# Kernel tuning notes

Hardware: AMD Instinct MI355X
Metric: run time of the kernel (lower is better)

The kernel has to match this reference:

```python
import jax, jax.numpy as jnp
import numpy as np

B, NSP, H, W = 8, 1024, 256, 256   # frames, superpixels/frame, label-map size
N = B * NSP                        # total superpixel nodes
MIX = 0.5                          # mixing_coeff
SIGMA = 0.05


def _interp_axis(x, out, axis):
    # 1-D bilinear interpolation along `axis`, align_corners=True
    n = x.shape[axis]
    pos = jnp.linspace(0.0, n - 1.0, out).astype(x.dtype)
    i0 = jnp.floor(pos).astype(jnp.int32)
    i1 = jnp.minimum(i0 + 1, n - 1)
    wt = pos - i0.astype(x.dtype)
    shp = [1] * x.ndim
    shp[axis] = out
    wt = wt.reshape(shp)
    return jnp.take(x, i0, axis=axis) * (1 - wt) + jnp.take(x, i1, axis=axis) * wt


def _upsample_ac(x, oh, ow):
    # nn.UpsamplingBilinear2d (align_corners=True)
    if x.shape[2] == oh and x.shape[3] == ow:
        return x
    return _interp_axis(_interp_axis(x, oh, 2), ow, 3)


def _sp_pool(feats, seg):
    # upsample [B,C,h,w] to label resolution, then average features per superpixel -> [N, C]
    C = feats.shape[1]
    up = _upsample_ac(feats, H, W)
    vals = up.transpose(0, 2, 3, 1).reshape(-1, C)          # [B*H*W, C]
    sums = jax.ops.segment_sum(vals, seg, num_segments=N)
    cnt = jax.ops.segment_sum(jnp.ones((seg.shape[0],), vals.dtype), seg, num_segments=N)
    return sums / jnp.maximum(cnt, 1.0)[:, None]


def _gcn(x, Wm, b, src, dst, ew):
    # GCNConv(normalize=False): out_i = sum_{j->i} ew * (x_j @ W) + b
    h = x @ Wm
    agg = jax.ops.segment_sum(h[src] * ew[:, None], dst, num_segments=x.shape[0])
    return agg + b


def _coord_map():
    # channel 0 varies along dim2 (w), channel 1 varies along dim3 (h), both in [0,1]
    c0 = jnp.broadcast_to((jnp.arange(H, dtype=jnp.float32) / (H - 1))[:, None], (H, W))
    c1 = jnp.broadcast_to((jnp.arange(W, dtype=jnp.float32) / (W - 1))[None, :], (H, W))
    return jnp.broadcast_to(jnp.stack([c0, c1], 0)[None], (B, 2, H, W))


def setup_inputs() -> dict:
    key = jax.random.key(0)
    ks = jax.random.split(key, 12)
    labels = jax.random.randint(ks[0], (B, 1, H, W), 0, NSP, dtype=jnp.int32)
    skip0 = jax.random.normal(ks[1], (B, 512, 32, 32), jnp.float32)
    skip1 = jax.random.normal(ks[2], (B, 256, 64, 64), jnp.float32)
    skip2 = jax.random.normal(ks[3], (B, 256, 128, 128), jnp.float32)
    E = 131072
    edges_nn = jax.random.randint(ks[4], (2, E), 0, N, dtype=jnp.int32)
    negs = jax.random.randint(ks[5], (E,), 0, N, dtype=jnp.int32)
    W0 = jax.random.normal(ks[6], (512, 256), jnp.float32) / np.float32(np.sqrt(512))
    W1 = jax.random.normal(ks[7], (256, 256), jnp.float32) / np.float32(np.sqrt(256))
    W2 = jax.random.normal(ks[8], (256, 256), jnp.float32) / np.float32(np.sqrt(256))
    lin_w = jax.random.normal(ks[9], (256, 1), jnp.float32) / np.float32(np.sqrt(256))
    z = jnp.zeros((256,), jnp.float32)
    return {"labels": labels, "skip0": skip0, "skip1": skip1, "skip2": skip2,
            "edges_nn": edges_nn, "negs": negs,
            "W0": W0, "b0": z, "W1": W1, "b1": z, "W2": W2, "b2": z, "lin_w": lin_w}


def reference(labels, skip0, skip1, skip2, edges_nn, negs, W0, b0, W1, b1, W2, b2, lin_w):
    # per-pixel global superpixel id (offset per frame)
    seg = (labels.reshape(B, -1) + NSP * jnp.arange(B, dtype=labels.dtype)[:, None]).reshape(-1)
    src, dst = edges_nn[0], edges_nn[1]

    # pooled normalized coordinates per superpixel -> gaussian edge weights
    pc = _sp_pool(_coord_map(), seg)                        # [N, 2]
    dr = pc[src] - pc[dst]
    dist = jnp.linalg.norm(dr, axis=1)
    edge_attr = jnp.exp(-dist ** 2 / SIGMA)

    x = _sp_pool(skip0, seg)                                # [N, 512]
    layers = [(W0, b0, None), (W1, b1, skip1), (W2, b2, skip2)]
    for i, (Wm, b, sk) in enumerate(layers):
        if i > 0:
            x = (1 - MIX) * x + MIX * _sp_pool(sk, seg)
        x = jax.nn.relu(_gcn(x, Wm, b, src, dst, edge_attr))

    s = x @ lin_w                                           # [N, 1]
    dap = jax.nn.sigmoid(s[src] - s[dst])
    dan = jax.nn.sigmoid(s[src] - s[negs])
    return dan, dap, edge_attr
```

## Files before the change

kernel.cpp:

```cpp
#include <hip/hip_runtime.h>
#include <hip/hip_bf16.h>
#include <cstdint>
#include <cstddef>

#define BB 8
#define NSPX 1024
#define NNODE 8192
#define EE 131072
#define NPIX 524288
#define CH 256

using bf16 = __hip_bfloat16;
typedef unsigned int uint;
typedef unsigned long long u64;

__device__ __forceinline__ float blo(uint u) { return __uint_as_float(u << 16); }
__device__ __forceinline__ float bhi(uint u) { return __uint_as_float(u & 0xffff0000u); }
__device__ __forceinline__ uint packbf2(float a, float b) {
  __hip_bfloat162 h = __float22bfloat162_rn(make_float2(a, b));
  return *reinterpret_cast<uint*>(&h);
}

__global__ __launch_bounds__(256) void zero_kernel(int4* p, int n4) {
  int i = blockIdx.x * 256 + threadIdx.x;
  int stride = gridDim.x * 256;
  int4 z = make_int4(0, 0, 0, 0);
  for (; i < n4; i += stride) p[i] = z;
}

__global__ __launch_bounds__(256) void cnt2_kernel(const int* __restrict__ labels,
                                                   const int* __restrict__ edst,
                                                   int* __restrict__ segb,
                                                   u64* __restrict__ packed,
                                                   int* __restrict__ cnt_e) {
  int blk = blockIdx.x;
  int t = threadIdx.x;
  if (blk < 2048) {
    int p = blk * 256 + t;
    int b = p >> 16;
    int h = (p >> 8) & 255;
    int w = p & 255;
    int seg = labels[p] + (b << 10);
    segb[p] = seg;
    u64 enc = (1ULL << 48) | ((u64)h << 24) | (u64)w;
    atomicAdd(&packed[seg], enc);
  } else {
    int e = (blk - 2048) * 256 + t;
    atomicAdd(&cnt_e[edst[e]], 1);
  }
}

__global__ __launch_bounds__(1024) void scan2_kernel(const u64* __restrict__ packed,
                                                     const int* __restrict__ cnt_e,
                                                     int* __restrict__ poff, int* __restrict__ eoff) {
  __shared__ int ps[1024];
  int which = blockIdx.x;
  int* coff = which ? eoff : poff;
  int t = threadIdx.x;
  int base = t * 8;
  int v[8];
  int sum = 0;
#pragma unroll
  for (int i = 0; i < 8; ++i) {
    int x = which ? cnt_e[base + i] : (int)(packed[base + i] >> 48);
    v[i] = sum;
    sum += x;
  }
  ps[t] = sum;
  __syncthreads();
  for (int off = 1; off < 1024; off <<= 1) {
    int x = (t >= off) ? ps[t - off] : 0;
    __syncthreads();
    ps[t] += x;
    __syncthreads();
  }
  int prev = (t == 0) ? 0 : ps[t - 1];
#pragma unroll
  for (int i = 0; i < 8; ++i) coff[base + i] = prev + v[i];
  if (t == 1023) coff[8192] = ps[1023];
}

__global__ __launch_bounds__(256) void rcnt_kernel(const u64* __restrict__ packed,
                                                   float* __restrict__ rcnt,
                                                   float* __restrict__ pch, float* __restrict__ pcw) {
  int n = blockIdx.x * 256 + threadIdx.x;
  if (n >= NNODE) return;
  u64 v = packed[n];
  int c = (int)(v >> 48);
  int sh = (int)((v >> 24) & 0xFFFFFF);
  int sw = (int)(v & 0xFFFFFF);
  float r = 1.0f / (float)(c > 1 ? c : 1);
  rcnt[n] = r;
  pch[n] = (float)sh * r * (1.0f / 255.0f);
  pcw[n] = (float)sw * r * (1.0f / 255.0f);
}

__global__ __launch_bounds__(256) void scatter2_kernel(const int* __restrict__ segb,
                                                       const int* __restrict__ poff,
                                                       int* __restrict__ pcur,
                                                       int* __restrict__ psorted,
                                                       const int* __restrict__ esrc,
                                                       const int* __restrict__ edst,
                                                       const float* __restrict__ pch,
                                                       const float* __restrict__ pcw,
                                                       const int* __restrict__ eoff,
                                                       int* __restrict__ ecur,
                                                       uint2* __restrict__ evw,
                                                       float* __restrict__ outp) {
  int blk = blockIdx.x;
  int t = threadIdx.x;
  if (blk < 2048) {
    int p = blk * 256 + t;
    int s = segb[p];
    int pos = poff[s] + atomicAdd(&pcur[s], 1);
    psorted[pos] = p;
  } else {
    int e = (blk - 2048) * 256 + t;
    int s1 = esrc[e], d1 = edst[e];
    float dh = pch[s1] - pch[d1];
    float dw = pcw[s1] - pcw[d1];
    float ea = expf(-(dh * dh + dw * dw) * 20.0f);
    outp[2 * EE + e] = ea;
    int pos = eoff[d1] + atomicAdd(&ecur[d1], 1);
    evw[pos] = make_uint2((uint)s1, __float_as_uint(ea));
  }
}

__global__ __launch_bounds__(256) void gemm_kmaj_bf16(const float* __restrict__ A,
                                                      const float* __restrict__ W,
                                                      bf16* __restrict__ out) {
  __shared__ float As[64][36];
  int b = blockIdx.z;
  int m0 = blockIdx.x * 32;
  int n0 = blockIdx.y * 128;
  int t = threadIdx.x;
  int ct = t & 31;
  int rm = t >> 5;
  int l8 = t & 7, kr = t >> 3;
  const float* Ab = A + (size_t)b * 512 * 1024;
  float4 acc[4];
#pragma unroll
  for (int i = 0; i < 4; ++i) acc[i] = make_float4(0.f, 0.f, 0.f, 0.f);
  for (int k0 = 0; k0 < 512; k0 += 64) {
#pragma unroll
    for (int pass = 0; pass < 2; ++pass) {
      int k = kr + pass * 32;
      float4 v = *(const float4*)&Ab[(size_t)(k0 + k) * 1024 + m0 + l8 * 4];
      *(float4*)&As[k][l8 * 4] = v;
    }
    __syncthreads();
#pragma unroll 8
    for (int k = 0; k < 64; ++k) {
      float4 a = *(const float4*)&As[k][rm * 4];
      float4 wv = *(const float4*)&W[(size_t)(k0 + k) * 256 + n0 + ct * 4];
      acc[0].x += a.x * wv.x; acc[0].y += a.x * wv.y; acc[0].z += a.x * wv.z; acc[0].w += a.x * wv.w;
      acc[1].x += a.y * wv.x; acc[1].y += a.y * wv.y; acc[1].z += a.y * wv.z; acc[1].w += a.y * wv.w;
      acc[2].x += a.z * wv.x; acc[2].y += a.z * wv.y; acc[2].z += a.z * wv.z; acc[2].w += a.z * wv.w;
      acc[3].x += a.w * wv.x; acc[3].y += a.w * wv.y; acc[3].z += a.w * wv.z; acc[3].w += a.w * wv.w;
    }
    __syncthreads();
  }
#pragma unroll
  for (int i = 0; i < 4; ++i) {
    int m = m0 + rm * 4 + i;
    uint2 pk = make_uint2(packbf2(acc[i].x, acc[i].y), packbf2(acc[i].z, acc[i].w));
    *(uint2*)&out[((size_t)b * 1024 + m) * 256 + n0 + ct * 4] = pk;
  }
}

__global__ __launch_bounds__(256) void transpose64_bf16(const float* __restrict__ src, bf16* __restrict__ dst,
                                                        int C, int P) {
  __shared__ float tile[64][65];
  int b = blockIdx.z;
  int p0 = blockIdx.x * 64;
  int c0 = blockIdx.y * 64;
  int t = threadIdx.x;
  int l16 = t & 15, r16 = t >> 4;
#pragma unroll
  for (int pass = 0; pass < 4; ++pass) {
    int c = r16 + pass * 16;
    float4 v = *(const float4*)&src[((size_t)b * C + c0 + c) * P + p0 + l16 * 4];
    tile[c][l16 * 4 + 0] = v.x;
    tile[c][l16 * 4 + 1] = v.y;
    tile[c][l16 * 4 + 2] = v.z;
    tile[c][l16 * 4 + 3] = v.w;
  }
  __syncthreads();
  int l8 = t & 7, r32 = t >> 3;
#pragma unroll
  for (int pass = 0; pass < 2; ++pass) {
    int p = r32 + pass * 32;
    uint r[4];
#pragma unroll
    for (int q = 0; q < 4; ++q)
      r[q] = packbf2(tile[l8 * 8 + 2 * q][p], tile[l8 * 8 + 2 * q + 1][p]);
    *(uint4*)&dst[((size_t)b * P + p0 + p) * C + c0 + l8 * 8] = make_uint4(r[0], r[1], r[2], r[3]);
  }
}

__device__ __forceinline__ void accum8(float wt, uint4 u, float* a) {
  a[0] += wt * blo(u.x); a[1] += wt * bhi(u.x);
  a[2] += wt * blo(u.y); a[3] += wt * bhi(u.y);
  a[4] += wt * blo(u.z); a[5] += wt * bhi(u.z);
  a[6] += wt * blo(u.w); a[7] += wt * bhi(u.w);
}

template <int HS>
__device__ __forceinline__ void taps_scale(const bf16* __restrict__ fb, int h, int w, float* acc) {
  const float fh = (float)(HS - 1) / 255.0f;
  float ph = h * fh, pw = w * fh;
  int i0 = (int)ph, j0 = (int)pw;
  float th = ph - (float)i0, tw = pw - (float)j0;
  int i1 = min(i0 + 1, HS - 1), jj1 = min(j0 + 1, HS - 1);
  float w11 = th * tw, w10 = th - w11, w01 = tw - w11, w00 = 1.f - th - tw + w11;
  uint4 u00 = *(const uint4*)(fb + (i0 * HS + j0) * 256);
  uint4 u01 = *(const uint4*)(fb + (i0 * HS + jj1) * 256);
  uint4 u10 = *(const uint4*)(fb + (i1 * HS + j0) * 256);
  uint4 u11 = *(const uint4*)(fb + (i1 * HS + jj1) * 256);
  accum8(w00, u00, acc);
  accum8(w01, u01, acc);
  accum8(w10, u10, acc);
  accum8(w11, u11, acc);
}

__global__ __launch_bounds__(256) void gather01_kernel(const bf16* __restrict__ F0,
                                                       const bf16* __restrict__ F1,
                                                       const int* __restrict__ poff,
                                                       const int* __restrict__ psorted,
                                                       const float* __restrict__ rc,
                                                       bf16* __restrict__ p0out,
                                                       float* __restrict__ p1out) {
  int blk = blockIdx.x;
  int n = ((blk & 7) << 10) | (blk >> 3);
  int b = n >> 10;
  int t = threadIdx.x;
  int l = t & 31;
  int s = t >> 5;
  const bf16* f0 = F0 + (size_t)b * 1024 * 256 + l * 8;
  const bf16* f1 = F1 + (size_t)b * 4096 * 256 + l * 8;
  int j1 = poff[n + 1];
  float a0[8], a1[8];
#pragma unroll
  for (int i = 0; i < 8; ++i) { a0[i] = 0.f; a1[i] = 0.f; }
  for (int j = poff[n] + s; j < j1; j += 8) {
    int p = psorted[j];
    int h = (p >> 8) & 255, w = p & 255;
    taps_scale<32>(f0, h, w, a0);
    taps_scale<64>(f1, h, w, a1);
  }
  __shared__ float4 red[2][512];
  red[0][t * 2 + 0] = make_float4(a0[0], a0[1], a0[2], a0[3]);
  red[0][t * 2 + 1] = make_float4(a0[4], a0[5], a0[6], a0[7]);
  red[1][t * 2 + 0] = make_float4(a1[0], a1[1], a1[2], a1[3]);
  red[1][t * 2 + 1] = make_float4(a1[4], a1[5], a1[6], a1[7]);
  __syncthreads();
  if (t < 64) {
    float r = rc[n];
    int l2 = t >> 1, half = t & 1;
    float4 s0 = make_float4(0.f, 0.f, 0.f, 0.f), s1 = s0;
#pragma unroll
    for (int ss = 0; ss < 8; ++ss) {
      float4 v0 = red[0][(ss * 32 + l2) * 2 + half];
      float4 v1 = red[1][(ss * 32 + l2) * 2 + half];
      s0.x += v0.x; s0.y += v0.y; s0.z += v0.z; s0.w += v0.w;
      s1.x += v1.x; s1.y += v1.y; s1.z += v1.z; s1.w += v1.w;
    }
    s0.x *= r; s0.y *= r; s0.z *= r; s0.w *= r;
    s1.x *= r; s1.y *= r; s1.z *= r; s1.w *= r;
    *(uint2*)&p0out[(size_t)n * 256 + 4 * t] = make_uint2(packbf2(s0.x, s0.y), packbf2(s0.z, s0.w));
    *(float4*)&p1out[(size_t)n * 256 + 4 * t] = s1;
  }
}

__global__ __launch_bounds__(256) void gather2_kernel(const bf16* __restrict__ F,
                                                      const int* __restrict__ poff,
                                                      const int* __restrict__ psorted,
                                                      const float* __restrict__ rc,
                                                      float* __restrict__ pout) {
  int blk = blockIdx.x;
  int n = ((blk & 7) << 10) | (blk >> 3);
  int b = n >> 10;
  int c0 = blockIdx.y * 128;
  int t = threadIdx.x;
  int l = t & 15;
  int s = t >> 4;
  const bf16* fb = F + (size_t)b * 16384 * 256 + c0 + l * 8;
  int j1 = poff[n + 1];
  float acc[8];
#pragma unroll
  for (int i = 0; i < 8; ++i) acc[i] = 0.f;
  for (int j = poff[n] + s; j < j1; j += 16) {
    int p = psorted[j];
    int h = (p >> 8) & 255, w = p & 255;
    taps_scale<128>(fb, h, w, acc);
  }
  __shared__ float4 red4[512];
  red4[t * 2 + 0] = make_float4(acc[0], acc[1], acc[2], acc[3]);
  red4[t * 2 + 1] = make_float4(acc[4], acc[5], acc[6], acc[7]);
  __syncthreads();
  if (t < 32) {
    float r = rc[n];
    int l2 = t >> 1, half = t & 1;
    float4 sum = make_float4(0.f, 0.f, 0.f, 0.f);
#pragma unroll
    for (int ss = 0; ss < 16; ++ss) {
      float4 v = red4[(ss * 16 + l2) * 2 + half];
      sum.x += v.x; sum.y += v.y; sum.z += v.z; sum.w += v.w;
    }
    sum.x *= r; sum.y *= r; sum.z *= r; sum.w *= r;
    *(float4*)&pout[(size_t)n * 256 + c0 + t * 4] = sum;
  }
}

__global__ __launch_bounds__(256) void gemm_mix_n256(const float* __restrict__ X, const float* __restrict__ Pl,
                                                     const float* __restrict__ W, bf16* __restrict__ out) {
  const int t = threadIdx.x;
  const int r0 = blockIdx.x * 16;
  const int cw = (t & 63) * 4;
  const int rg = (t >> 6) * 4;
  __shared__ float Xl[16][68];
  float4 acc[4];
#pragma unroll
  for (int i = 0; i < 4; ++i) acc[i] = make_float4(0.f, 0.f, 0.f, 0.f);
  for (int k0 = 0; k0 < 256; k0 += 64) {
#pragma unroll
    for (int l = 0; l < 4; ++l) {
      int idx = t + 256 * l;
      int r = idx >> 6, k = idx & 63;
      size_t a = (size_t)(r0 + r) * 256 + k0 + k;
      Xl[r][k] = 0.5f * (X[a] + Pl[a]);
    }
    __syncthreads();
#pragma unroll
    for (int k4 = 0; k4 < 64; k4 += 4) {
      float4 a[4];
#pragma unroll
      for (int i = 0; i < 4; ++i) a[i] = *(const float4*)&Xl[rg + i][k4];
#pragma unroll
      for (int kk = 0; kk < 4; ++kk) {
        float4 w = *(const float4*)&W[(size_t)(k0 + k4 + kk) * 256 + cw];
#pragma unroll
        for (int i = 0; i < 4; ++i) {
          float av = ((const float*)&a[i])[kk];
          acc[i].x += av * w.x;
          acc[i].y += av * w.y;
          acc[i].z += av * w.z;
          acc[i].w += av * w.w;
        }
      }
    }
    __syncthreads();
  }
#pragma unroll
  for (int i = 0; i < 4; ++i) {
    uint2 pk = make_uint2(packbf2(acc[i].x, acc[i].y), packbf2(acc[i].z, acc[i].w));
    *(uint2*)&out[(size_t)(r0 + rg + i) * 256 + cw] = pk;
  }
}

__global__ __launch_bounds__(256) void agg_kernel(const bf16* __restrict__ h, const float* __restrict__ bias,
                                                  const int* __restrict__ eoff,
                                                  const uint2* __restrict__ evw,
                                                  float* __restrict__ xout) {
  int n = blockIdx.x * 2 + (threadIdx.x >> 7);
  int c2 = threadIdx.x & 127;
  int e0 = eoff[n], e1 = eoff[n + 1];
  float a0 = 0.f, a1 = 0.f;
  for (int j = e0; j < e1; ++j) {
    uint2 ev = evw[j];
    float wv = __uint_as_float(ev.y);
    uint hv = *(const uint*)&h[((size_t)ev.x << 8) + c2 * 2];
    a0 += wv * blo(hv);
    a1 += wv * bhi(hv);
  }
  float v0 = a0 + bias[2 * c2];
  float v1 = a1 + bias[2 * c2 + 1];
  float2 st = make_float2(v0 > 0.f ? v0 : 0.f, v1 > 0.f ? v1 : 0.f);
  *(float2*)&xout[((size_t)n << 8) + 2 * c2] = st;
}

__global__ __launch_bounds__(256) void score_kernel(const float* __restrict__ x, const float* __restrict__ lw,
                                                    float* __restrict__ s) {
  int t = threadIdx.x;
  int n = blockIdx.x * 4 + (t >> 6);
  int lane = t & 63;
  const float* row = x + ((size_t)n << 8);
  float v = row[lane] * lw[lane] + row[lane + 64] * lw[lane + 64] +
            row[lane + 128] * lw[lane + 128] + row[lane + 192] * lw[lane + 192];
#pragma unroll
  for (int off = 32; off > 0; off >>= 1) v += __shfl_down(v, off, 64);
  if (lane == 0) s[n] = v;
}

__global__ __launch_bounds__(256) void out_kernel(const float* __restrict__ s, const int* __restrict__ src,
                                                  const int* __restrict__ dst, const int* __restrict__ negs,
                                                  float* __restrict__ outp) {
  int e = blockIdx.x * 256 + threadIdx.x;
  if (e >= EE) return;
  float ss = s[src[e]];
  float a = ss - s[negs[e]];
  float b = ss - s[dst[e]];
  outp[e] = 1.0f / (1.0f + expf(-a));
  outp[EE + e] = 1.0f / (1.0f + expf(-b));
}

extern "C" void kernel_launch(void* const* d_in, const int* in_sizes, int n_in,
                              void* d_out, int out_size, void* d_ws, size_t ws_size,
                              hipStream_t stream) {
  const int*   labels = (const int*)d_in[0];
  const float* skip0  = (const float*)d_in[1];
  const float* skip1  = (const float*)d_in[2];
  const float* skip2  = (const float*)d_in[3];
  const int*   edges  = (const int*)d_in[4];
  const int*   negs   = (const int*)d_in[5];
  const float* W0     = (const float*)d_in[6];
  const float* b0     = (const float*)d_in[7];
  const float* W1     = (const float*)d_in[8];
  const float* b1     = (const float*)d_in[9];
  const float* W2     = (const float*)d_in[10];
  const float* b2     = (const float*)d_in[11];
  const float* lw     = (const float*)d_in[12];
  const int* esrc = edges;
  const int* edst = edges + EE;
  float* outp = (float*)d_out;

  size_t o = 0;
  char* base = (char*)d_ws;
  auto alloc = [&](size_t bytes) -> void* {
    void* p = base + o;
    o += (bytes + 255) & ~(size_t)255;
    return p;
  };
  u64* packed  = (u64*)alloc(NNODE * 8);
  int* cnt_e   = (int*)alloc(NNODE * 4);
  int* ecur    = (int*)alloc(NNODE * 4);
  int* pcur    = (int*)alloc(NNODE * 4);
  size_t zbytes = o;
  float* rcnt    = (float*)alloc(NNODE * 4);
  float* pch     = (float*)alloc(NNODE * 4);
  float* pcw     = (float*)alloc(NNODE * 4);
  int*   poff    = (int*)alloc((NNODE + 1) * 4);
  int*   eoff    = (int*)alloc((NNODE + 1) * 4);
  uint2* evw     = (uint2*)alloc((size_t)EE * 8);
  int*   psorted = (int*)alloc(NPIX * 4);
  int*   segb    = (int*)alloc(NPIX * 4);
  float* bufA    = (float*)alloc((size_t)NNODE * CH * 4);
  float* bufB    = (float*)alloc((size_t)NNODE * CH * 4);
  float* p1buf   = (float*)alloc((size_t)NNODE * CH * 4);
  float* p2buf   = (float*)alloc((size_t)NNODE * CH * 4);
  bf16*  h0b     = (bf16*)alloc((size_t)NNODE * CH * 2);
  bf16*  h1b     = (bf16*)alloc((size_t)NNODE * CH * 2);
  bf16*  F0b     = (bf16*)alloc((size_t)BB * 1024 * CH * 2);
  bf16*  F1t     = (bf16*)alloc((size_t)BB * 4096 * CH * 2);
  bf16*  F2t     = (bf16*)alloc((size_t)BB * 16384 * CH * 2);
  float* sbuf    = (float*)alloc(NNODE * 4);
  (void)ws_size; (void)n_in; (void)in_sizes; (void)out_size;

  zero_kernel<<<64, 256, 0, stream>>>((int4*)d_ws, (int)(zbytes / 16));
  cnt2_kernel<<<2048 + 512, 256, 0, stream>>>(labels, edst, segb, packed, cnt_e);
  scan2_kernel<<<2, 1024, 0, stream>>>(packed, cnt_e, poff, eoff);
  rcnt_kernel<<<NNODE / 256, 256, 0, stream>>>(packed, rcnt, pch, pcw);
  scatter2_kernel<<<2048 + 512, 256, 0, stream>>>(segb, poff, pcur, psorted,
                                                  esrc, edst, pch, pcw, eoff, ecur, evw, outp);
  gemm_kmaj_bf16<<<dim3(32, 2, BB), 256, 0, stream>>>(skip0, W0, F0b);
  transpose64_bf16<<<dim3(4096 / 64, 4, BB), 256, 0, stream>>>(skip1, F1t, 256, 4096);
  transpose64_bf16<<<dim3(16384 / 64, 4, BB), 256, 0, stream>>>(skip2, F2t, 256, 16384);
  gather01_kernel<<<NNODE, 256, 0, stream>>>(F0b, F1t, poff, psorted, rcnt, h0b, p1buf);
  gather2_kernel<<<dim3(NNODE, 2), 256, 0, stream>>>(F2t, poff, psorted, rcnt, p2buf);
  agg_kernel<<<NNODE / 2, 256, 0, stream>>>(h0b, b0, eoff, evw, bufB);
  gemm_mix_n256<<<NNODE / 16, 256, 0, stream>>>(bufB, p1buf, W1, h1b);
  agg_kernel<<<NNODE / 2, 256, 0, stream>>>(h1b, b1, eoff, evw, bufA);
  gemm_mix_n256<<<NNODE / 16, 256, 0, stream>>>(bufA, p2buf, W2, h1b);
  agg_kernel<<<NNODE / 2, 256, 0, stream>>>(h1b, b2, eoff, evw, bufB);
  score_kernel<<<NNODE / 4, 256, 0, stream>>>(bufB, lw, sbuf);
  out_kernel<<<EE / 256, 256, 0, stream>>>(sbuf, esrc, edst, negs, outp);
}
```

Measured before the change: 738.0 us.

## Switch intermediate feature storage to fp16 and accumulate gathers with packed half FMA

Intermediate feature maps and GCN hidden states move from bf16 to fp16 storage. The bilinear-tap gather kernels now accumulate in packed __half2 with hfma2 and read 16 channels per thread, halving the threads per pixel and doubling the pixels processed in parallel. The goal is fewer ALU instructions per tap and wider loads. The cost is reduced accumulation precision: fp16 partial sums over many pixels may lose accuracy or overflow for large values.

```diff
diff --git a/kernel.cpp b/kernel.cpp
--- a/kernel.cpp
+++ b/kernel.cpp
@@ -1,5 +1,5 @@
 #include <hip/hip_runtime.h>
-#include <hip/hip_bf16.h>
+#include <hip/hip_fp16.h>
 #include <cstdint>
 #include <cstddef>
 
@@ -10,16 +10,15 @@
 #define NPIX 524288
 #define CH 256
 
-using bf16 = __hip_bfloat16;
 typedef unsigned int uint;
 typedef unsigned long long u64;
 
-__device__ __forceinline__ float blo(uint u) { return __uint_as_float(u << 16); }
-__device__ __forceinline__ float bhi(uint u) { return __uint_as_float(u & 0xffff0000u); }
-__device__ __forceinline__ uint packbf2(float a, float b) {
-  __hip_bfloat162 h = __float22bfloat162_rn(make_float2(a, b));
+__device__ __forceinline__ uint packh2(float a, float b) {
+  __half2 h = __float22half2_rn(make_float2(a, b));
   return *reinterpret_cast<uint*>(&h);
 }
+__device__ __forceinline__ __half2 uh2(uint u) { return *reinterpret_cast<__half2*>(&u); }
+__device__ __forceinline__ uint h2u(__half2 h) { return *reinterpret_cast<uint*>(&h); }
 
 __global__ __launch_bounds__(256) void zero_kernel(int4* p, int n4) {
   int i = blockIdx.x * 256 + threadIdx.x;
@@ -126,9 +125,9 @@
   }
 }
 
-__global__ __launch_bounds__(256) void gemm_kmaj_bf16(const float* __restrict__ A,
-                                                      const float* __restrict__ W,
-                                                      bf16* __restrict__ out) {
+__global__ __launch_bounds__(256) void gemm_kmaj_f16(const float* __restrict__ A,
+                                                     const float* __restrict__ W,
+                                                     __half* __restrict__ out) {
   __shared__ float As[64][36];
   int b = blockIdx.z;
   int m0 = blockIdx.x * 32;
@@ -163,13 +162,13 @@
 #pragma unroll
   for (int i = 0; i < 4; ++i) {
     int m = m0 + rm * 4 + i;
-    uint2 pk = make_uint2(packbf2(acc[i].x, acc[i].y), packbf2(acc[i].z, acc[i].w));
+    uint2 pk = make_uint2(packh2(acc[i].x, acc[i].y), packh2(acc[i].z, acc[i].w));
     *(uint2*)&out[((size_t)b * 1024 + m) * 256 + n0 + ct * 4] = pk;
   }
 }
 
-__global__ __launch_bounds__(256) void transpose64_bf16(const float* __restrict__ src, bf16* __restrict__ dst,
-                                                        int C, int P) {
+__global__ __launch_bounds__(256) void transpose64_f16(const float* __restrict__ src, __half* __restrict__ dst,
+                                                       int C, int P) {
   __shared__ float tile[64][65];
   int b = blockIdx.z;
   int p0 = blockIdx.x * 64;
@@ -193,86 +192,87 @@
     uint r[4];
 #pragma unroll
     for (int q = 0; q < 4; ++q)
-      r[q] = packbf2(tile[l8 * 8 + 2 * q][p], tile[l8 * 8 + 2 * q + 1][p]);
+      r[q] = packh2(tile[l8 * 8 + 2 * q][p], tile[l8 * 8 + 2 * q + 1][p]);
     *(uint4*)&dst[((size_t)b * P + p0 + p) * C + c0 + l8 * 8] = make_uint4(r[0], r[1], r[2], r[3]);
   }
 }
 
-__device__ __forceinline__ void accum8(float wt, uint4 u, float* a) {
-  a[0] += wt * blo(u.x); a[1] += wt * bhi(u.x);
-  a[2] += wt * blo(u.y); a[3] += wt * bhi(u.y);
-  a[4] += wt * blo(u.z); a[5] += wt * bhi(u.z);
-  a[6] += wt * blo(u.w); a[7] += wt * bhi(u.w);
+__device__ __forceinline__ void tap16(const __half* __restrict__ tp, float wt, __half2* acc) {
+  uint4 qa = *(const uint4*)tp;
+  uint4 qb = *(const uint4*)(tp + 8);
+  __half2 W = __float2half2_rn(wt);
+  acc[0] = __hfma2(W, uh2(qa.x), acc[0]);
+  acc[1] = __hfma2(W, uh2(qa.y), acc[1]);
+  acc[2] = __hfma2(W, uh2(qa.z), acc[2]);
+  acc[3] = __hfma2(W, uh2(qa.w), acc[3]);
+  acc[4] = __hfma2(W, uh2(qb.x), acc[4]);
+  acc[5] = __hfma2(W, uh2(qb.y), acc[5]);
+  acc[6] = __hfma2(W, uh2(qb.z), acc[6]);
+  acc[7] = __hfma2(W, uh2(qb.w), acc[7]);
 }
 
 template <int HS>
-__device__ __forceinline__ void taps_scale(const bf16* __restrict__ fb, int h, int w, float* acc) {
+__device__ __forceinline__ void taps16(const __half* __restrict__ fb, int h, int w, __half2* acc) {
   const float fh = (float)(HS - 1) / 255.0f;
   float ph = h * fh, pw = w * fh;
   int i0 = (int)ph, j0 = (int)pw;
   float th = ph - (float)i0, tw = pw - (float)j0;
   int i1 = min(i0 + 1, HS - 1), jj1 = min(j0 + 1, HS - 1);
   float w11 = th * tw, w10 = th - w11, w01 = tw - w11, w00 = 1.f - th - tw + w11;
-  uint4 u00 = *(const uint4*)(fb + (i0 * HS + j0) * 256);
-  uint4 u01 = *(const uint4*)(fb + (i0 * HS + jj1) * 256);
-  uint4 u10 = *(const uint4*)(fb + (i1 * HS + j0) * 256);
-  uint4 u11 = *(const uint4*)(fb + (i1 * HS + jj1) * 256);
-  accum8(w00, u00, acc);
-  accum8(w01, u01, acc);
-  accum8(w10, u10, acc);
-  accum8(w11, u11, acc);
-}
-
-__global__ __launch_bounds__(256) void gather01_kernel(const bf16* __restrict__ F0,
-                                                       const bf16* __restrict__ F1,
+  tap16(fb + (i0 * HS + j0) * 256, w00, acc);
+  tap16(fb + (i0 * HS + jj1) * 256, w01, acc);
+  tap16(fb + (i1 * HS + j0) * 256, w10, acc);
+  tap16(fb + (i1 * HS + jj1) * 256, w11, acc);
+}
+
+__global__ __launch_bounds__(256) void gather01_kernel(const __half* __restrict__ F0,
+                                                       const __half* __restrict__ F1,
                                                        const int* __restrict__ poff,
                                                        const int* __restrict__ psorted,
                                                        const float* __restrict__ rc,
-                                                       bf16* __restrict__ p0out,
+                                                       __half* __restrict__ p0out,
                                                        float* __restrict__ p1out) {
   int blk = blockIdx.x;
   int n = ((blk & 7) << 10) | (blk >> 3);
   int b = n >> 10;
   int t = threadIdx.x;
-  int l = t & 31;
-  int s = t >> 5;
-  const bf16* f0 = F0 + (size_t)b * 1024 * 256 + l * 8;
-  const bf16* f1 = F1 + (size_t)b * 4096 * 256 + l * 8;
+  int l = t & 15;
+  int s = t >> 4;
+  const __half* f0 = F0 + (size_t)b * 1024 * 256 + l * 16;
+  const __half* f1 = F1 + (size_t)b * 4096 * 256 + l * 16;
   int j1 = poff[n + 1];
-  float a0[8], a1[8];
-#pragma unroll
-  for (int i = 0; i < 8; ++i) { a0[i] = 0.f; a1[i] = 0.f; }
-  for (int j = poff[n] + s; j < j1; j += 8) {
+  __half2 z = __float2half2_rn(0.f);
+  __half2 a0[8], a1[8];
+#pragma unroll
+  for (int i = 0; i < 8; ++i) { a0[i] = z; a1[i] = z; }
+  for (int j = poff[n] + s; j < j1; j += 16) {
     int p = psorted[j];
     int h = (p >> 8) & 255, w = p & 255;
-    taps_scale<32>(f0, h, w, a0);
-    taps_scale<64>(f1, h, w, a1);
-  }
-  __shared__ float4 red[2][512];
-  red[0][t * 2 + 0] = make_float4(a0[0], a0[1], a0[2], a0[3]);
-  red[0][t * 2 + 1] = make_float4(a0[4], a0[5], a0[6], a0[7]);
-  red[1][t * 2 + 0] = make_float4(a1[0], a1[1], a1[2], a1[3]);
-  red[1][t * 2 + 1] = make_float4(a1[4], a1[5], a1[6], a1[7]);
+    taps16<32>(f0, h, w, a0);
+    taps16<64>(f1, h, w, a1);
+  }
+  __shared__ uint red[2][256][9];
+#pragma unroll
+  for (int k = 0; k < 8; ++k) { red[0][t][k] = h2u(a0[k]); red[1][t][k] = h2u(a1[k]); }
   __syncthreads();
-  if (t < 64) {
+  if (t < 128) {
+    int l2 = t >> 3, k = t & 7;
     float r = rc[n];
-    int l2 = t >> 1, half = t & 1;
-    float4 s0 = make_float4(0.f, 0.f, 0.f, 0.f), s1 = s0;
-#pragma unroll
-    for (int ss = 0; ss < 8; ++ss) {
-      float4 v0 = red[0][(ss * 32 + l2) * 2 + half];
-      float4 v1 = red[1][(ss * 32 + l2) * 2 + half];
-      s0.x += v0.x; s0.y += v0.y; s0.z += v0.z; s0.w += v0.w;
-      s1.x += v1.x; s1.y += v1.y; s1.z += v1.z; s1.w += v1.w;
-    }
-    s0.x *= r; s0.y *= r; s0.z *= r; s0.w *= r;
-    s1.x *= r; s1.y *= r; s1.z *= r; s1.w *= r;
-    *(uint2*)&p0out[(size_t)n * 256 + 4 * t] = make_uint2(packbf2(s0.x, s0.y), packbf2(s0.z, s0.w));
-    *(float4*)&p1out[(size_t)n * 256 + 4 * t] = s1;
-  }
-}
-
-__global__ __launch_bounds__(256) void gather2_kernel(const bf16* __restrict__ F,
+    float2 s0 = make_float2(0.f, 0.f), s1 = s0;
+#pragma unroll
+    for (int ss = 0; ss < 16; ++ss) {
+      float2 v0 = __half22float2(uh2(red[0][ss * 16 + l2][k]));
+      float2 v1 = __half22float2(uh2(red[1][ss * 16 + l2][k]));
+      s0.x += v0.x; s0.y += v0.y;
+      s1.x += v1.x; s1.y += v1.y;
+    }
+    int c = l2 * 16 + k * 2;
+    *(uint*)&p0out[(size_t)n * 256 + c] = packh2(s0.x * r, s0.y * r);
+    *(float2*)&p1out[(size_t)n * 256 + c] = make_float2(s1.x * r, s1.y * r);
+  }
+}
+
+__global__ __launch_bounds__(256) void gather2_kernel(const __half* __restrict__ F,
                                                       const int* __restrict__ poff,
                                                       const int* __restrict__ psorted,
                                                       const float* __restrict__ rc,
@@ -282,38 +282,39 @@
   int b = n >> 10;
   int c0 = blockIdx.y * 128;
   int t = threadIdx.x;
-  int l = t & 15;
-  int s = t >> 4;
-  const bf16* fb = F + (size_t)b * 16384 * 256 + c0 + l * 8;
+  int l = t & 7;
+  int s = t >> 3;
+  const __half* fb = F + (size_t)b * 16384 * 256 + c0 + l * 16;
   int j1 = poff[n + 1];
-  float acc[8];
-#pragma unroll
-  for (int i = 0; i < 8; ++i) acc[i] = 0.f;
-  for (int j = poff[n] + s; j < j1; j += 16) {
+  __half2 z = __float2half2_rn(0.f);
+  __half2 acc[8];
+#pragma unroll
+  for (int i = 0; i < 8; ++i) acc[i] = z;
+  for (int j = poff[n] + s; j < j1; j += 32) {
     int p = psorted[j];
     int h = (p >> 8) & 255, w = p & 255;
-    taps_scale<128>(fb, h, w, acc);
-  }
-  __shared__ float4 red4[512];
-  red4[t * 2 + 0] = make_float4(acc[0], acc[1], acc[2], acc[3]);
-  red4[t * 2 + 1] = make_float4(acc[4], acc[5], acc[6], acc[7]);
+    taps16<128>(fb, h, w, acc);
+  }
+  __shared__ uint red[256][9];
+#pragma unroll
+  for (int k = 0; k < 8; ++k) red[t][k] = h2u(acc[k]);
   __syncthreads();
-  if (t < 32) {
+  if (t < 64) {
+    int l2 = t >> 3, k = t & 7;
     float r = rc[n];
-    int l2 = t >> 1, half = t & 1;
-    float4 sum = make_float4(0.f, 0.f, 0.f, 0.f);
-#pragma unroll
-    for (int ss = 0; ss < 16; ++ss) {
-      float4 v = red4[(ss * 16 + l2) * 2 + half];
-      sum.x += v.x; sum.y += v.y; sum.z += v.z; sum.w += v.w;
-    }
-    sum.x *= r; sum.y *= r; sum.z *= r; sum.w *= r;
-    *(float4*)&pout[(size_t)n * 256 + c0 + t * 4] = sum;
+    float2 sm = make_float2(0.f, 0.f);
+#pragma unroll
+    for (int ss = 0; ss < 32; ++ss) {
+      float2 v = __half22float2(uh2(red[ss * 8 + l2][k]));
+      sm.x += v.x; sm.y += v.y;
+    }
+    int c = c0 + l2 * 16 + k * 2;
+    *(float2*)&pout[(size_t)n * 256 + c] = make_float2(sm.x * r, sm.y * r);
   }
 }
 
 __global__ __launch_bounds__(256) void gemm_mix_n256(const float* __restrict__ X, const float* __restrict__ Pl,
-                                                     const float* __restrict__ W, bf16* __restrict__ out) {
+                                                     const float* __restrict__ W, __half* __restrict__ out) {
   const int t = threadIdx.x;
   const int r0 = blockIdx.x * 16;
   const int cw = (t & 63) * 4;
@@ -353,12 +354,12 @@
   }
 #pragma unroll
   for (int i = 0; i < 4; ++i) {
-    uint2 pk = make_uint2(packbf2(acc[i].x, acc[i].y), packbf2(acc[i].z, acc[i].w));
+    uint2 pk = make_uint2(packh2(acc[i].x, acc[i].y), packh2(acc[i].z, acc[i].w));
     *(uint2*)&out[(size_t)(r0 + rg + i) * 256 + cw] = pk;
   }
 }
 
-__global__ __launch_bounds__(256) void agg_kernel(const bf16* __restrict__ h, const float* __restrict__ bias,
+__global__ __launch_bounds__(256) void agg_kernel(const __half* __restrict__ h, const float* __restrict__ bias,
                                                   const int* __restrict__ eoff,
                                                   const uint2* __restrict__ evw,
                                                   float* __restrict__ xout) {
@@ -370,8 +371,9 @@
     uint2 ev = evw[j];
     float wv = __uint_as_float(ev.y);
     uint hv = *(const uint*)&h[((size_t)ev.x << 8) + c2 * 2];
-    a0 += wv * blo(hv);
-    a1 += wv * bhi(hv);
+    float2 f = __half22float2(uh2(hv));
+    a0 += wv * f.x;
+    a1 += wv * f.y;
   }
   float v0 = a0 + bias[2 * c2];
   float v1 = a1 + bias[2 * c2 + 1];
@@ -436,24 +438,24 @@
   int* ecur    = (int*)alloc(NNODE * 4);
   int* pcur    = (int*)alloc(NNODE * 4);
   size_t zbytes = o;
-  float* rcnt    = (float*)alloc(NNODE * 4);
-  float* pch     = (float*)alloc(NNODE * 4);
-  float* pcw     = (float*)alloc(NNODE * 4);
-  int*   poff    = (int*)alloc((NNODE + 1) * 4);
-  int*   eoff    = (int*)alloc((NNODE + 1) * 4);
-  uint2* evw     = (uint2*)alloc((size_t)EE * 8);
-  int*   psorted = (int*)alloc(NPIX * 4);
-  int*   segb    = (int*)alloc(NPIX * 4);
-  float* bufA    = (float*)alloc((size_t)NNODE * CH * 4);
-  float* bufB    = (float*)alloc((size_t)NNODE * CH * 4);
-  float* p1buf   = (float*)alloc((size_t)NNODE * CH * 4);
-  float* p2buf   = (float*)alloc((size_t)NNODE * CH * 4);
-  bf16*  h0b     = (bf16*)alloc((size_t)NNODE * CH * 2);
-  bf16*  h1b     = (bf16*)alloc((size_t)NNODE * CH * 2);
-  bf16*  F0b     = (bf16*)alloc((size_t)BB * 1024 * CH * 2);
-  bf16*  F1t     = (bf16*)alloc((size_t)BB * 4096 * CH * 2);
-  bf16*  F2t     = (bf16*)alloc((size_t)BB * 16384 * CH * 2);
-  float* sbuf    = (float*)alloc(NNODE * 4);
+  float*  rcnt    = (float*)alloc(NNODE * 4);
+  float*  pch     = (float*)alloc(NNODE * 4);
+  float*  pcw     = (float*)alloc(NNODE * 4);
+  int*    poff    = (int*)alloc((NNODE + 1) * 4);
+  int*    eoff    = (int*)alloc((NNODE + 1) * 4);
+  uint2*  evw     = (uint2*)alloc((size_t)EE * 8);
+  int*    psorted = (int*)alloc(NPIX * 4);
+  int*    segb    = (int*)alloc(NPIX * 4);
+  float*  bufA    = (float*)alloc((size_t)NNODE * CH * 4);
+  float*  bufB    = (float*)alloc((size_t)NNODE * CH * 4);
+  float*  p1buf   = (float*)alloc((size_t)NNODE * CH * 4);
+  float*  p2buf   = (float*)alloc((size_t)NNODE * CH * 4);
+  __half* h0b     = (__half*)alloc((size_t)NNODE * CH * 2);
+  __half* h1b     = (__half*)alloc((size_t)NNODE * CH * 2);
+  __half* F0b     = (__half*)alloc((size_t)BB * 1024 * CH * 2);
+  __half* F1t     = (__half*)alloc((size_t)BB * 4096 * CH * 2);
+  __half* F2t     = (__half*)alloc((size_t)BB * 16384 * CH * 2);
+  float*  sbuf    = (float*)alloc(NNODE * 4);
   (void)ws_size; (void)n_in; (void)in_sizes; (void)out_size;
 
   zero_kernel<<<64, 256, 0, stream>>>((int4*)d_ws, (int)(zbytes / 16));
@@ -462,9 +464,9 @@
   rcnt_kernel<<<NNODE / 256, 256, 0, stream>>>(packed, rcnt, pch, pcw);
   scatter2_kernel<<<2048 + 512, 256, 0, stream>>>(segb, poff, pcur, psorted,
                                                   esrc, edst, pch, pcw, eoff, ecur, evw, outp);
-  gemm_kmaj_bf16<<<dim3(32, 2, BB), 256, 0, stream>>>(skip0, W0, F0b);
-  transpose64_bf16<<<dim3(4096 / 64, 4, BB), 256, 0, stream>>>(skip1, F1t, 256, 4096);
-  transpose64_bf16<<<dim3(16384 / 64, 4, BB), 256, 0, stream>>>(skip2, F2t, 256, 16384);
+  gemm_kmaj_f16<<<dim3(32, 2, BB), 256, 0, stream>>>(skip0, W0, F0b);
+  transpose64_f16<<<dim3(4096 / 64, 4, BB), 256, 0, stream>>>(skip1, F1t, 256, 4096);
+  transpose64_f16<<<dim3(16384 / 64, 4, BB), 256, 0, stream>>>(skip2, F2t, 256, 16384);
   gather01_kernel<<<NNODE, 256, 0, stream>>>(F0b, F1t, poff, psorted, rcnt, h0b, p1buf);
   gather2_kernel<<<dim3(NNODE, 2), 256, 0, stream>>>(F2t, poff, psorted, rcnt, p2buf);
   agg_kernel<<<NNODE / 2, 256, 0, stream>>>(h0b, b0, eoff, evw, bufB);
```

Measured after the change: 728.3 us. Within noise of the previous version (-1.3%).
